# Optimization experiments

Measured on AMD Instinct MI355X. Metric: run time of the kernel, lower is better.

The kernel has to match this reference:

```python
import jax, jax.numpy as jnp
import numpy as np
from jax import lax

MU = 0.1          # cfg MODEL.MU (FISTA step size)
LMBD = 0.1        # cfg MODEL.LAMBDA[0]
N_STEPS = 4       # cfg MODEL.NUM_LAYERS (unrolled FISTA iterations)
BN_EPS = 1e-5


def _norm_w(W):
    # DictBlock w_norm: each dictionary filter normalized to unit L2 norm.
    # torch does this under no_grad (in-place on .data), so the norm is a constant.
    n = jnp.sqrt(jnp.sum(W * W, axis=(1, 2, 3), keepdims=True))
    return W / lax.stop_gradient(n + 1e-12)


def _conv(x, W, stride, pad):
    return lax.conv_general_dilated(x, W, (stride, stride), [(pad, pad)] * 2,
                                    dimension_numbers=('NCHW', 'OIHW', 'NCHW'))


def _conv_t(z, W, stride, pad, out_pad):
    # torch conv_transpose2d(z, W, stride, padding=pad, output_padding=out_pad)
    k = W.shape[2]
    Wt = jnp.transpose(jnp.flip(W, (2, 3)), (1, 0, 2, 3))  # (in_ch, dict, k, k)
    p = k - 1 - pad
    return lax.conv_general_dilated(z, Wt, (1, 1), [(p, p + out_pad)] * 2,
                                    lhs_dilation=(stride, stride),
                                    dimension_numbers=('NCHW', 'OIHW', 'NCHW'))


def _shrink(c):
    # non-negative soft threshold: relu(c - lmbd*step)
    return jax.nn.relu(c - LMBD * MU)


def _dict_conv(x, W, stride):
    # Unrolled FISTA sparse coding: min_c 0.5||x - W^T c||^2 + lmbd||c||_1, c>=0
    W = _norm_w(W)
    out_pad = stride - 1
    c = _shrink(MU * _conv(x, W, stride, 1))
    c_pre = jnp.zeros_like(c)
    t = 1.0
    for _ in range(N_STEPS - 1):
        t_next = (1.0 + float(np.sqrt(1.0 + 4.0 * t * t))) / 2.0
        a = c + ((t - 1.0) / t_next) * (c - c_pre)
        c_pre = c
        r = x - _conv_t(a, W, stride, 1, out_pad)       # reconstruction residual
        c = _shrink(a + MU * _conv(r, W, stride, 1))    # proximal gradient step
        t = t_next
    return c


def _bn(x, g, b, m, v):
    # eval-mode BatchNorm2d with running stats
    scale = g * lax.rsqrt(v + BN_EPS)
    return (x - m[None, :, None, None]) * scale[None, :, None, None] + b[None, :, None, None]


def setup_inputs() -> dict:
    key = jax.random.key(0)
    ks = jax.random.split(key, 12)
    N, Cin, Cout, H = 32, 128, 256, 56
    x = jax.random.normal(ks[0], (N, Cin, H, H), jnp.float32)
    def unit_norm(W):
        return W / (jnp.sqrt(jnp.sum(W * W, axis=(1, 2, 3), keepdims=True)) + 1e-12)
    W1 = unit_norm(jax.random.normal(ks[1], (Cout, Cin, 3, 3), jnp.float32))
    W2 = unit_norm(jax.random.normal(ks[2], (Cout, Cout, 3, 3), jnp.float32))
    Wsc = jax.random.normal(ks[3], (Cout, Cin, 1, 1), jnp.float32) * 0.05
    def bn(k):
        k1, k2, k3, k4 = jax.random.split(k, 4)
        g = 1.0 + 0.1 * jax.random.normal(k1, (Cout,), jnp.float32)
        b = 0.1 * jax.random.normal(k2, (Cout,), jnp.float32)
        m = 0.1 * jax.random.normal(k3, (Cout,), jnp.float32)
        v = 0.5 + jax.random.uniform(k4, (Cout,), jnp.float32)
        return g, b, m, v
    bn1_g, bn1_b, bn1_m, bn1_v = bn(ks[4])
    bn2_g, bn2_b, bn2_m, bn2_v = bn(ks[5])
    bnsc_g, bnsc_b, bnsc_m, bnsc_v = bn(ks[6])
    return dict(x=x, W1=W1, W2=W2, Wsc=Wsc,
                bn1_g=bn1_g, bn1_b=bn1_b, bn1_m=bn1_m, bn1_v=bn1_v,
                bn2_g=bn2_g, bn2_b=bn2_b, bn2_m=bn2_m, bn2_v=bn2_v,
                bnsc_g=bnsc_g, bnsc_b=bnsc_b, bnsc_m=bnsc_m, bnsc_v=bnsc_v)


def reference(x, W1, W2, Wsc,
              bn1_g, bn1_b, bn1_m, bn1_v,
              bn2_g, bn2_b, bn2_m, bn2_v,
              bnsc_g, bnsc_b, bnsc_m, bnsc_v):
    out = _bn(_dict_conv(x, W1, 2), bn1_g, bn1_b, bn1_m, bn1_v)
    out = _bn(_dict_conv(out, W2, 1), bn2_g, bn2_b, bn2_m, bn2_v)
    sc = _bn(_conv(x, Wsc, 2, 0), bnsc_g, bnsc_b, bnsc_m, bnsc_v)
    return jax.nn.relu(out + sc)
```

## Files before the change

### kernel.cpp

```cpp
#include <hip/hip_runtime.h>
#include <math.h>

#define MU_F 0.1f
#define SHRINK_F 0.01f
#define BN_EPS_F 1e-5f

typedef _Float16 half_t;
typedef _Float16 half8 __attribute__((ext_vector_type(8)));
typedef float f32x4 __attribute__((ext_vector_type(4)));

__device__ __forceinline__ void gll16(const half_t* g, half_t* l) {
    __builtin_amdgcn_global_load_lds(
        (const __attribute__((address_space(1))) void*)g,
        (__attribute__((address_space(3))) void*)l, 16, 0, 0);
}

#define VM_WAIT_BARRIER(N) do {                                   \
    asm volatile("s_waitcnt vmcnt(" #N ")" ::: "memory");         \
    __builtin_amdgcn_s_barrier();                                 \
    __builtin_amdgcn_sched_barrier(0);                            \
} while (0)

template<int KS, int S, int PAD, int MODE>
__global__ __launch_bounds__(256, 2)
void conv_big(const half_t* __restrict__ Ag, const half_t* __restrict__ Xh,
              float* __restrict__ outF, half_t* __restrict__ outH,
              const half_t* __restrict__ auxH, const float* __restrict__ auxF,
              int CA, int Cout, int Hin, int Win, int Hout, int Wout, int ptiles,
              float alpha, float beta, float delta, int relu1,
              const float* __restrict__ pscale, const float* __restrict__ pbias,
              const float* __restrict__ aux3, int relu2,
              const half_t* __restrict__ zpg, int edge_defer,
              float* __restrict__ out2F)
{
    __shared__ __align__(16) half_t sm[4 * 8192];

    const int tid = threadIdx.x;
    const int wv = tid >> 6, ln = tid & 63;
    const int co0 = blockIdx.y * 128;
    const int wco = (wv & 1) * 64, wpx = (wv >> 1) * 64;

    int bx;
    {
        const int nwg = gridDim.x;
        const int q = nwg >> 3, r8 = nwg & 7;
        const int xcd = blockIdx.x & 7, idx = blockIdx.x >> 3;
        bx = (xcd < r8 ? xcd * (q + 1) : r8 * (q + 1) + (xcd - r8) * q) + idx;
    }
    const int p0 = bx * 128;
    (void)ptiles;

    const int PHW1 = Hout * Wout;
    const int NPX  = PHW1 * 32;
    const int K9   = KS * KS * CA;

    const int r  = tid >> 2;
    const int s4 = tid & 3;
    const int sw = (s4 ^ ((r >> 1) & 3)) << 3;

    const size_t abase0 = (size_t)(co0 + r     ) * K9;
    const size_t abase1 = (size_t)(co0 + r + 64) * K9;

    int bph[2], bpw[2]; bool bval[2]; size_t bnb[2];
#pragma unroll
    for (int i = 0; i < 2; ++i) {
        int px = p0 + i * 64 + r;
        bval[i] = px < NPX;
        int pc = bval[i] ? px : 0;
        int n2 = pc / PHW1; int rem = pc - n2 * PHW1;
        int ph = rem / Wout;
        bph[i] = ph; bpw[i] = rem - ph * Wout;
        bnb[i] = (size_t)n2 * Hin * Win;
    }

    const int cpt = CA >> 5;
    const int lgc = (cpt == 8) ? 3 : 2;
    const int ntap = KS * KS;
    const int total = ntap << lgc;

    auto issue = [&](int flat, half_t* dst) {
        const int ci = flat & (cpt - 1);
        const int ti = flat >> lgc;
        int kh, kw;
        if (KS == 3) {
            kh = (ti * 11) >> 5; kw = ti - 3 * kh;
        } else { kh = 0; kw = 0; }
        const int c0 = ci << 5;
        const size_t koff = (size_t)(kh * KS + kw) * CA + c0 + sw;
        gll16(Ag + abase0 + koff, dst +        tid * 8);
        gll16(Ag + abase1 + koff, dst + 2048 + tid * 8);
#pragma unroll
        for (int i = 0; i < 2; ++i) {
            int hh, ww2; bool ok = bval[i];
            if (MODE == 0) {
                hh = bph[i] * S - PAD + kh; ww2 = bpw[i] * S - PAD + kw;
                ok = ok && (unsigned)hh < (unsigned)Hin && (unsigned)ww2 < (unsigned)Win;
            } else {
                hh = bph[i] + PAD - kh; ww2 = bpw[i] + PAD - kw;
                ok = ok && (unsigned)hh < (unsigned)Hin && (unsigned)ww2 < (unsigned)Win;
            }
            const half_t* src = ok
                ? Xh + (bnb[i] + (size_t)(hh * Win + ww2)) * CA + c0 + sw
                : zpg;
            gll16(src, dst + 4096 + i * 2048 + tid * 8);
        }
    };

    f32x4 acc[4][4] = {};

    issue(0, sm);
    issue(1, sm + 8192);
    issue(2, sm + 16384);
    VM_WAIT_BARRIER(8);

    const int fr = ln & 15, q8 = ln >> 4;
    const int sx = (q8 ^ ((fr >> 1) & 3)) << 3;
    const int rdA = (wco + fr) * 32 + sx;
    const int rdB = (128 + wpx + fr) * 32 + sx;

    for (int k = 0; k < total; ++k) {
        half_t* bufr = sm + (k & 3) * 8192;
        if (k + 3 < total)
            issue(k + 3, sm + ((k + 3) & 3) * 8192);
        half8 fa[4], fb[4];
#pragma unroll
        for (int m = 0; m < 4; ++m)
            fa[m] = *(const half8*)(bufr + rdA + m * 512);
#pragma unroll
        for (int t2 = 0; t2 < 4; ++t2)
            fb[t2] = *(const half8*)(bufr + rdB + t2 * 512);
#pragma unroll
        for (int m = 0; m < 4; ++m)
#pragma unroll
            for (int t2 = 0; t2 < 4; ++t2)
                acc[m][t2] = __builtin_amdgcn_mfma_f32_16x16x32_f16(fa[m], fb[t2], acc[m][t2], 0, 0, 0);
        if (k + 3 < total)      VM_WAIT_BARRIER(8);
        else if (k + 2 < total) VM_WAIT_BARRIER(4);
        else if (k + 1 < total) VM_WAIT_BARRIER(0);
    }

    const int rg = ln >> 4;
#pragma unroll
    for (int t = 0; t < 4; ++t) {
        int px = p0 + wpx + t * 16 + fr;
        if (px >= NPX) continue;
        int n2 = px / PHW1; int rem = px - n2 * PHW1;
        int oh = rem / Wout, ow = rem - oh * Wout;
        size_t ghwc = ((size_t)(n2 * Hout + oh) * Wout + ow) * Cout;
        bool defer = edge_defer && (oh == 0 || ow == 0);
#pragma unroll
        for (int m = 0; m < 4; ++m) {
#pragma unroll
            for (int rr = 0; rr < 4; ++rr) {
                int co_l = co0 + wco + m * 16 + rg * 4 + rr;
                size_t fidx = ((size_t)(n2 * Cout + co_l) * Hout + oh) * Wout + ow;
                float av = alpha * acc[m][t][rr];
                if (out2F) out2F[fidx] = av;
                float v = av + delta;
                if (auxH) v += beta * (float)auxH[ghwc + co_l];
                if (auxF) v += beta * auxF[fidx];
                if (!defer) {
                    if (relu1) v = fmaxf(v, 0.f);
                    if (pscale) v = pscale[co_l] * v + pbias[co_l];
                    if (aux3) v += aux3[fidx];
                    if (relu2) v = fmaxf(v, 0.f);
                }
                if (outH) outH[ghwc + co_l] = (half_t)v;
                else      outF[fidx] = v;
            }
        }
    }
}

template<int KT>
__global__ __launch_bounds__(256)
void pack_w(const float* __restrict__ W, half_t* __restrict__ Wh,
            half_t* __restrict__ WTh, int Cin, int Cout, int do_norm)
{
    __shared__ float red[256];
    int co = blockIdx.x, tid = threadIdx.x;
    int CK = Cin * KT;
    const float* w = W + (size_t)co * CK;
    float inv = 1.f;
    if (do_norm) {
        float s = 0.f;
        for (int i = tid; i < CK; i += 256) { float v = w[i]; s += v * v; }
        red[tid] = s; __syncthreads();
        for (int o = 128; o > 0; o >>= 1) {
            if (tid < o) red[tid] += red[tid + o];
            __syncthreads();
        }
        inv = 1.f / (sqrtf(red[0]) + 1e-12f);
    }
    for (int i = tid; i < CK; i += 256) {
        int ci = i / KT, tap = i - ci * KT;
        half_t h = (half_t)(w[i] * inv);
        Wh[((size_t)co * KT + tap) * Cin + ci] = h;
        if (WTh) WTh[((size_t)ci * KT + tap) * Cout + co] = h;
    }
}

__global__ __launch_bounds__(256)
void gram_kernel(const half_t* __restrict__ Wh, half_t* __restrict__ Gp,
                 half_t* __restrict__ ChT, half_t* __restrict__ CwT,
                 half_t* __restrict__ CcT)
{
    __shared__ float Wa[9 * 128];
    int co = blockIdx.x, b = threadIdx.x;
    for (int i = b; i < 9 * 128; i += 256) Wa[i] = (float)Wh[(size_t)co * 9 * 128 + i];
    __syncthreads();
    const half_t* Wb = Wh + (size_t)b * 9 * 128;
    auto dot = [&](int tA, int tB) {
        float s = 0.f;
        for (int c = 0; c < 128; ++c) s += Wa[tA * 128 + c] * (float)Wb[tB * 128 + c];
        return s;
    };
    auto lo = [](int t) { return (t == 2) ? 2 : 0; };
    auto hi = [](int t) { return (t == 1) ? 3 : ((t == 2) ? 3 : 1); };
    for (int th = 0; th < 3; ++th)
        for (int tw = 0; tw < 3; ++tw) {
            float s = 0.f;
            for (int kh = lo(th); kh < hi(th); ++kh)
                for (int kw = lo(tw); kw < hi(tw); ++kw)
                    s += dot(kh * 3 + kw, (kh + 2 - 2 * th) * 3 + (kw + 2 - 2 * tw));
            Gp[((size_t)co * 9 + th * 3 + tw) * 256 + b] = (half_t)s;
        }
    for (int tw = 0; tw < 3; ++tw) {
        float s = 0.f, s2 = 0.f;
        for (int k = lo(tw); k < hi(tw); ++k) {
            s  += dot(k, k + 2 - 2 * tw);
            s2 += dot(k * 3, (k + 2 - 2 * tw) * 3);
        }
        ChT[((size_t)tw * 256 + b) * 256 + co] = (half_t)s;
        CwT[((size_t)tw * 256 + b) * 256 + co] = (half_t)s2;
    }
    CcT[(size_t)b * 256 + co] = (half_t)dot(0, 0);
}

__global__ __launch_bounds__(256)
void edge_fix(const half_t* __restrict__ a, half_t* out,
              const half_t* __restrict__ ChT, const half_t* __restrict__ CwT,
              const half_t* __restrict__ CcT,
              const float* __restrict__ ps, const float* __restrict__ pb)
{
    int i = blockIdx.x, n = blockIdx.y, co = threadIdx.x;
    int oh, ow;
    if (i < 28) { oh = 0; ow = i; } else { oh = i - 27; ow = 0; }
    float corr = 0.f;
    if (oh == 0) {
        for (int kw = 0; kw < 3; ++kw) {
            int pw = ow - 1 + kw;
            if ((unsigned)pw < 28u) {
                const half_t* ap = a + ((size_t)(n * 28 + 0) * 28 + pw) * 256;
                const half_t* cp = ChT + (size_t)kw * 256 * 256 + co;
                for (int b2 = 0; b2 < 256; ++b2)
                    corr += (float)cp[(size_t)b2 * 256] * (float)ap[b2];
            }
        }
    }
    if (ow == 0) {
        for (int kh = 0; kh < 3; ++kh) {
            int ph = oh - 1 + kh;
            if ((unsigned)ph < 28u) {
                const half_t* ap = a + ((size_t)(n * 28 + ph) * 28 + 0) * 256;
                const half_t* cp = CwT + (size_t)kh * 256 * 256 + co;
                for (int b2 = 0; b2 < 256; ++b2)
                    corr += (float)cp[(size_t)b2 * 256] * (float)ap[b2];
            }
        }
    }
    if (oh == 0 && ow == 0) {
        const half_t* ap = a + ((size_t)(n * 28) * 28) * 256;
        for (int b2 = 0; b2 < 256; ++b2)
            corr -= (float)CcT[(size_t)b2 * 256 + co] * (float)ap[b2];
    }
    size_t idx = ((size_t)(n * 28 + oh) * 28 + ow) * 256 + co;
    float v = (float)out[idx] + MU_F * corr;
    v = fmaxf(v, 0.f);
    if (ps) v = ps[co] * v + pb[co];
    out[idx] = (half_t)v;
}

__global__ __launch_bounds__(256)
void tx_kernel(const float* __restrict__ x, half_t* __restrict__ xTh)
{
    __shared__ __align__(16) half_t tl[56 * 136];
    int h = blockIdx.x, n = blockIdx.y, tid = threadIdx.x;
    for (int it = 0; it < 28; ++it) {
        int id = tid + it * 256;
        int c = id / 56, w0 = id - c * 56;
        tl[w0 * 136 + c] = (half_t)x[(((size_t)n * 128 + c) * 56 + h) * 56 + w0];
    }
    __syncthreads();
    if (tid < 224) {
        int w0 = tid >> 2, part = tid & 3;
        size_t base = (((size_t)n * 56 + h) * 56 + w0) * 128 + part * 32;
#pragma unroll
        for (int j = 0; j < 4; ++j)
            *(half8*)(xTh + base + j * 8) = *(const half8*)(tl + w0 * 136 + part * 32 + j * 8);
    }
}

__global__ __launch_bounds__(256)
void comb_kernel(const half_t* __restrict__ c, const half_t* __restrict__ p,
                 half_t* __restrict__ a, float w1, float w2, int n8)
{
    int i = blockIdx.x * 256 + threadIdx.x;
    if (i >= n8) return;
    half8 cv = ((const half8*)c)[i];
    half8 pv = ((const half8*)p)[i];
    half8 rres;
#pragma unroll
    for (int j = 0; j < 8; ++j) rres[j] = (half_t)(w1 * (float)cv[j] + w2 * (float)pv[j]);
    ((half8*)a)[i] = rres;
}

__global__ __launch_bounds__(256)
void bn_prep_kernel(const float* __restrict__ g, const float* __restrict__ b,
                    const float* __restrict__ m, const float* __restrict__ v,
                    float* __restrict__ s, float* __restrict__ t, int C)
{
    int i = blockIdx.x * 256 + threadIdx.x;
    if (i < C) {
        float sc = g[i] * rsqrtf(v[i] + BN_EPS_F);
        s[i] = sc; t[i] = b[i] - m[i] * sc;
    }
}

__global__ __launch_bounds__(128)
void zfill_kernel(half_t* __restrict__ p)
{
    p[threadIdx.x] = (half_t)0.f;
}

extern "C" void kernel_launch(void* const* d_in, const int* in_sizes, int n_in,
                              void* d_out, int out_size, void* d_ws, size_t ws_size,
                              hipStream_t stream)
{
    (void)in_sizes; (void)n_in; (void)out_size;
    const float* x    = (const float*)d_in[0];
    const float* W1   = (const float*)d_in[1];
    const float* W2   = (const float*)d_in[2];
    const float* Wsc  = (const float*)d_in[3];
    const float* bn1g = (const float*)d_in[4];
    const float* bn1b = (const float*)d_in[5];
    const float* bn1m = (const float*)d_in[6];
    const float* bn1v = (const float*)d_in[7];
    const float* bn2g = (const float*)d_in[8];
    const float* bn2b = (const float*)d_in[9];
    const float* bn2m = (const float*)d_in[10];
    const float* bn2v = (const float*)d_in[11];
    const float* bscg = (const float*)d_in[12];
    const float* bscb = (const float*)d_in[13];
    const float* bscm = (const float*)d_in[14];
    const float* bscv = (const float*)d_in[15];

    const size_t NB = (size_t)32 * 256 * 28 * 28;
    const size_t NX = (size_t)32 * 128 * 56 * 56;

    char* base = (char*)d_ws;
    size_t off = 0;
    auto alloc = [&](size_t nbytes) -> void* {
        void* r = base + off;
        off = (off + nbytes + 255) & ~(size_t)255;
        return r;
    };
    half_t* Wh1  = (half_t*)alloc(294912 * 2);
    half_t* WTh1 = (half_t*)alloc(294912 * 2);
    half_t* Wh2  = (half_t*)alloc(589824 * 2);
    half_t* WTh2 = (half_t*)alloc(589824 * 2);
    half_t* Wsch = (half_t*)alloc(32768 * 2);
    half_t* Gph  = (half_t*)alloc(589824 * 2);
    half_t* ChT  = (half_t*)alloc(196608 * 2);
    half_t* CwT  = (half_t*)alloc(196608 * 2);
    half_t* CcT  = (half_t*)alloc(65536 * 2);
    float* bn1s = (float*)alloc(256 * 4);  float* bn1t = (float*)alloc(256 * 4);
    float* bn2s = (float*)alloc(256 * 4);  float* bn2t = (float*)alloc(256 * 4);
    float* bscs = (float*)alloc(256 * 4);  float* bsct = (float*)alloc(256 * 4);
    half_t* zpg  = (half_t*)alloc(256);
    half_t* xTh  = (half_t*)alloc(NX * 2);
    half_t* Pa   = (half_t*)alloc(NB * 2);
    half_t* Pb   = (half_t*)alloc(NB * 2);
    half_t* Pc   = (half_t*)alloc(NB * 2);
    half_t* Py   = (half_t*)alloc(NB * 2);
    half_t* r28h = (half_t*)alloc(NB * 2);
    float*  scF  = (float*)alloc(NB * 4);
    if (off > ws_size) return;
    (void)WTh1;

    float*  cxF = (float*)Py;
    half_t* Pd  = (half_t*)xTh;

    float* outp = (float*)d_out;

    double t = 1.0; float al[3];
    for (int i = 0; i < 3; ++i) {
        double tn = (1.0 + sqrt(1.0 + 4.0 * t * t)) / 2.0;
        al[i] = (float)((t - 1.0) / tn); t = tn;
    }

    const dim3 blk(256);
    const dim3 cblk(256);
    const dim3 gB(196, 2, 1);
    const dim3 gE(55, 32, 1);
    const int n8 = (int)(NB / 8);
    const dim3 gC((n8 + 255) / 256);
    const float* NF = nullptr;
    const half_t* NH = nullptr;
    float* NFo = nullptr;
    half_t* NHo = nullptr;

    pack_w<9><<<256, blk, 0, stream>>>(W1, Wh1, nullptr, 128, 256, 1);
    pack_w<9><<<256, blk, 0, stream>>>(W2, Wh2, WTh2, 256, 256, 1);
    pack_w<1><<<256, blk, 0, stream>>>(Wsc, Wsch, nullptr, 128, 256, 0);
    gram_kernel<<<256, blk, 0, stream>>>(Wh1, Gph, ChT, CwT, CcT);
    bn_prep_kernel<<<1, blk, 0, stream>>>(bn1g, bn1b, bn1m, bn1v, bn1s, bn1t, 256);
    bn_prep_kernel<<<1, blk, 0, stream>>>(bn2g, bn2b, bn2m, bn2v, bn2s, bn2t, 256);
    bn_prep_kernel<<<1, blk, 0, stream>>>(bscg, bscb, bscm, bscv, bscs, bsct, 256);
    zfill_kernel<<<1, dim3(128), 0, stream>>>(zpg);
    tx_kernel<<<dim3(56, 32), blk, 0, stream>>>(x, xTh);

    conv_big<3,2,1,0><<<gB, cblk, 0, stream>>>(Wh1, xTh, NFo, Pa, NH, NF,
        128, 256, 56, 56, 28, 28, 196, MU_F, 0.f, -SHRINK_F, 1, NF, NF, NF, 0, zpg, 0, cxF);
    conv_big<1,2,0,0><<<gB, cblk, 0, stream>>>(Wsch, xTh, scF, NHo, NH, NF,
        128, 256, 56, 56, 28, 28, 196, 1.f, 0.f, 0.f, 0, bscs, bsct, NF, 0, zpg, 0, NFo);

    conv_big<3,1,1,0><<<gB, cblk, 0, stream>>>(Gph, Pa, NFo, Pb, Pa, cxF,
        256, 256, 28, 28, 28, 28, 196, -MU_F, 1.f, -SHRINK_F, 1, NF, NF, NF, 0, zpg, 1, NFo);
    edge_fix<<<gE, cblk, 0, stream>>>(Pa, Pb, ChT, CwT, CcT, NF, NF);

    comb_kernel<<<gC, blk, 0, stream>>>(Pb, Pa, Pc, 1.f + al[1], -al[1], n8);
    conv_big<3,1,1,0><<<gB, cblk, 0, stream>>>(Gph, Pc, NFo, Pa, Pc, cxF,
        256, 256, 28, 28, 28, 28, 196, -MU_F, 1.f, -SHRINK_F, 1, NF, NF, NF, 0, zpg, 1, NFo);
    edge_fix<<<gE, cblk, 0, stream>>>(Pc, Pa, ChT, CwT, CcT, NF, NF);

    comb_kernel<<<gC, blk, 0, stream>>>(Pa, Pb, Pc, 1.f + al[2], -al[2], n8);
    conv_big<3,1,1,0><<<gB, cblk, 0, stream>>>(Gph, Pc, NFo, Pb, Pc, cxF,
        256, 256, 28, 28, 28, 28, 196, -MU_F, 1.f, -SHRINK_F, 1, bn1s, bn1t, NF, 0, zpg, 1, NFo);
    edge_fix<<<gE, cblk, 0, stream>>>(Pc, Pb, ChT, CwT, CcT, bn1s, bn1t);

    conv_big<3,1,1,0><<<gB, cblk, 0, stream>>>(Wh2, Pb, NFo, Pa, NH, NF,
        256, 256, 28, 28, 28, 28, 196, MU_F, 0.f, -SHRINK_F, 1, NF, NF, NF, 0, zpg, 0, NFo);

    conv_big<3,1,1,1><<<gB, cblk, 0, stream>>>(WTh2, Pa, NFo, r28h, Pb, NF,
        256, 256, 28, 28, 28, 28, 196, -1.f, 1.f, 0.f, 0, NF, NF, NF, 0, zpg, 0, NFo);
    conv_big<3,1,1,0><<<gB, cblk, 0, stream>>>(Wh2, r28h, NFo, Pd, Pa, NF,
        256, 256, 28, 28, 28, 28, 196, MU_F, 1.f, -SHRINK_F, 1, NF, NF, NF, 0, zpg, 0, NFo);

    comb_kernel<<<gC, blk, 0, stream>>>(Pd, Pa, Pc, 1.f + al[1], -al[1], n8);
    conv_big<3,1,1,1><<<gB, cblk, 0, stream>>>(WTh2, Pc, NFo, r28h, Pb, NF,
        256, 256, 28, 28, 28, 28, 196, -1.f, 1.f, 0.f, 0, NF, NF, NF, 0, zpg, 0, NFo);
    conv_big<3,1,1,0><<<gB, cblk, 0, stream>>>(Wh2, r28h, NFo, Pa, Pc, NF,
        256, 256, 28, 28, 28, 28, 196, MU_F, 1.f, -SHRINK_F, 1, NF, NF, NF, 0, zpg, 0, NFo);

    comb_kernel<<<gC, blk, 0, stream>>>(Pa, Pd, Pc, 1.f + al[2], -al[2], n8);
    conv_big<3,1,1,1><<<gB, cblk, 0, stream>>>(WTh2, Pc, NFo, r28h, Pb, NF,
        256, 256, 28, 28, 28, 28, 196, -1.f, 1.f, 0.f, 0, NF, NF, NF, 0, zpg, 0, NFo);
    conv_big<3,1,1,0><<<gB, cblk, 0, stream>>>(Wh2, r28h, outp, NHo, Pc, NF,
        256, 256, 28, 28, 28, 28, 196, MU_F, 1.f, -SHRINK_F, 1, bn2s, bn2t, scF, 1, zpg, 0, NFo);
}
```

Measured before the change: 1.317 ms.

## Load activation operand directly to registers and repack weights into K-chunked layout

The conv GEMM kernel no longer stages the pixel (B) operand through shared memory. Each lane now gathers its half8 fragments straight from global memory into double-buffered registers, while only the weight (A) tile still goes through a 3-slot LDS ring. Weights and the Gram matrix are repacked into a [k-chunk][tap][cout][32] layout so each A tile is one contiguous block, and a separate raw-layout pack feeds the Gram computation. This cuts LDS use and barrier traffic per step, at the cost of uncoalesced per-lane global gathers and a shallower prefetch depth.

Result: slower. 1.623 ms (+23.3%).

```diff
diff --git a/kernel.cpp b/kernel.cpp
--- a/kernel.cpp
+++ b/kernel.cpp
@@ -33,12 +33,13 @@
               const half_t* __restrict__ zpg, int edge_defer,
               float* __restrict__ out2F)
 {
-    __shared__ __align__(16) half_t sm[4 * 8192];
+    __shared__ __align__(16) half_t sm[3 * 4096];
 
     const int tid = threadIdx.x;
     const int wv = tid >> 6, ln = tid & 63;
     const int co0 = blockIdx.y * 128;
     const int wco = (wv & 1) * 64, wpx = (wv >> 1) * 64;
+    (void)ptiles;
 
     int bx;
     {
@@ -48,104 +49,95 @@
         bx = (xcd < r8 ? xcd * (q + 1) : r8 * (q + 1) + (xcd - r8) * q) + idx;
     }
     const int p0 = bx * 128;
-    (void)ptiles;
 
     const int PHW1 = Hout * Wout;
     const int NPX  = PHW1 * 32;
-    const int K9   = KS * KS * CA;
-
-    const int r  = tid >> 2;
-    const int s4 = tid & 3;
-    const int sw = (s4 ^ ((r >> 1) & 3)) << 3;
-
-    const size_t abase0 = (size_t)(co0 + r     ) * K9;
-    const size_t abase1 = (size_t)(co0 + r + 64) * K9;
-
-    int bph[2], bpw[2]; bool bval[2]; size_t bnb[2];
-#pragma unroll
-    for (int i = 0; i < 2; ++i) {
-        int px = p0 + i * 64 + r;
-        bval[i] = px < NPX;
-        int pc = bval[i] ? px : 0;
-        int n2 = pc / PHW1; int rem = pc - n2 * PHW1;
-        int ph = rem / Wout;
-        bph[i] = ph; bpw[i] = rem - ph * Wout;
-        bnb[i] = (size_t)n2 * Hin * Win;
-    }
-
-    const int cpt = CA >> 5;
-    const int lgc = (cpt == 8) ? 3 : 2;
-    const int ntap = KS * KS;
-    const int total = ntap << lgc;
-
-    auto issue = [&](int flat, half_t* dst) {
-        const int ci = flat & (cpt - 1);
-        const int ti = flat >> lgc;
-        int kh, kw;
-        if (KS == 3) {
-            kh = (ti * 11) >> 5; kw = ti - 3 * kh;
-        } else { kh = 0; kw = 0; }
-        const int c0 = ci << 5;
-        const size_t koff = (size_t)(kh * KS + kw) * CA + c0 + sw;
-        gll16(Ag + abase0 + koff, dst +        tid * 8);
-        gll16(Ag + abase1 + koff, dst + 2048 + tid * 8);
-#pragma unroll
-        for (int i = 0; i < 2; ++i) {
-            int hh, ww2; bool ok = bval[i];
-            if (MODE == 0) {
-                hh = bph[i] * S - PAD + kh; ww2 = bpw[i] * S - PAD + kw;
-                ok = ok && (unsigned)hh < (unsigned)Hin && (unsigned)ww2 < (unsigned)Win;
-            } else {
-                hh = bph[i] + PAD - kh; ww2 = bpw[i] + PAD - kw;
-                ok = ok && (unsigned)hh < (unsigned)Hin && (unsigned)ww2 < (unsigned)Win;
-            }
-            const half_t* src = ok
-                ? Xh + (bnb[i] + (size_t)(hh * Win + ww2)) * CA + c0 + sw
-                : zpg;
-            gll16(src, dst + 4096 + i * 2048 + tid * 8);
-        }
+
+    const int r   = tid >> 2;
+    const int s4  = tid & 3;
+    const int asl = (s4 ^ ((r >> 1) & 3)) << 3;
+
+    const int fr = ln & 15, q8 = ln >> 4;
+    const int koh = q8 * 8;
+    const int sx  = (q8 ^ ((fr >> 1) & 3)) << 3;
+    const int rdA = (wco + fr) * 32 + sx;
+
+    const int cpt   = CA >> 5;
+    const int ntap  = KS * KS;
+    const int total = ntap * cpt;
+
+    int eph[4], epw[4], en2[4]; size_t ebase[4]; bool evalid[4];
+#pragma unroll
+    for (int t2 = 0; t2 < 4; ++t2) {
+        int px = p0 + wpx + t2 * 16 + fr;
+        evalid[t2] = px < NPX;
+        int pc = evalid[t2] ? px : 0;
+        en2[t2] = pc / PHW1; int rem = pc - en2[t2] * PHW1;
+        eph[t2] = rem / Wout; epw[t2] = rem - eph[t2] * Wout;
+        ebase[t2] = (size_t)en2[t2] * Hin * Win;
+    }
+
+    auto issueA = [&](int flat, half_t* dst) {
+        const size_t base = ((size_t)flat * Cout + co0) * 32;
+        gll16(Ag + base + (size_t)r * 32 + asl,        dst +        tid * 8);
+        gll16(Ag + base + (size_t)(r + 64) * 32 + asl, dst + 2048 + tid * 8);
     };
 
+    auto loadB = [&](int flat, half8 (&rb)[4]) {
+        int cc, ti;
+        if (KS == 1) { cc = flat; ti = 0; }
+        else         { cc = (flat * 57) >> 9; ti = flat - 9 * cc; }
+        const int kh = (KS == 3) ? ((ti * 11) >> 5) : 0;
+        const int kw = (KS == 3) ? (ti - 3 * kh) : 0;
+        const int c0h = (cc << 5) + koh;
+#pragma unroll
+        for (int t2 = 0; t2 < 4; ++t2) {
+            int ihh, iww; bool ok = evalid[t2];
+            if (MODE == 0) { ihh = eph[t2] * S - PAD + kh; iww = epw[t2] * S - PAD + kw; }
+            else           { ihh = eph[t2] + PAD - kh;     iww = epw[t2] + PAD - kw; }
+            ok = ok && (unsigned)ihh < (unsigned)Hin && (unsigned)iww < (unsigned)Win;
+            long long soff = ((long long)ebase[t2] + (long long)ihh * Win + iww) * CA + c0h;
+            const half_t* p = ok ? (Xh + soff) : zpg;
+            rb[t2] = *(const half8*)p;
+        }
+    };
+
     f32x4 acc[4][4] = {};
-
-    issue(0, sm);
-    issue(1, sm + 8192);
-    issue(2, sm + 16384);
-    VM_WAIT_BARRIER(8);
-
-    const int fr = ln & 15, q8 = ln >> 4;
-    const int sx = (q8 ^ ((fr >> 1) & 3)) << 3;
-    const int rdA = (wco + fr) * 32 + sx;
-    const int rdB = (128 + wpx + fr) * 32 + sx;
-
-    for (int k = 0; k < total; ++k) {
-        half_t* bufr = sm + (k & 3) * 8192;
-        if (k + 3 < total)
-            issue(k + 3, sm + ((k + 3) & 3) * 8192);
-        half8 fa[4], fb[4];
+    half8 rb0[4], rb1[4];
+
+    issueA(0, sm);
+    issueA(1, sm + 4096);
+    __builtin_amdgcn_sched_barrier(0);
+    loadB(0, rb0);
+    VM_WAIT_BARRIER(6);
+
+    auto step = [&](int k, half8 (&rbR)[4], half8 (&rbW)[4]) {
+        half_t* slot = sm + (k % 3) * 4096;
+        if (k + 2 < total) issueA(k + 2, sm + ((k + 2) % 3) * 4096);
+        __builtin_amdgcn_sched_barrier(0);
+        if (k + 1 < total) loadB(k + 1, rbW);
+        half8 fa[4];
 #pragma unroll
         for (int m = 0; m < 4; ++m)
-            fa[m] = *(const half8*)(bufr + rdA + m * 512);
-#pragma unroll
-        for (int t2 = 0; t2 < 4; ++t2)
-            fb[t2] = *(const half8*)(bufr + rdB + t2 * 512);
+            fa[m] = *(const half8*)(slot + rdA + m * 512);
 #pragma unroll
         for (int m = 0; m < 4; ++m)
 #pragma unroll
             for (int t2 = 0; t2 < 4; ++t2)
-                acc[m][t2] = __builtin_amdgcn_mfma_f32_16x16x32_f16(fa[m], fb[t2], acc[m][t2], 0, 0, 0);
-        if (k + 3 < total)      VM_WAIT_BARRIER(8);
-        else if (k + 2 < total) VM_WAIT_BARRIER(4);
-        else if (k + 1 < total) VM_WAIT_BARRIER(0);
+                acc[m][t2] = __builtin_amdgcn_mfma_f32_16x16x32_f16(fa[m], rbR[t2], acc[m][t2], 0, 0, 0);
+        if (k + 1 < total) VM_WAIT_BARRIER(6);
+    };
+
+    for (int k = 0; k < total; k += 2) {
+        step(k,     rb0, rb1);
+        step(k + 1, rb1, rb0);
     }
 
     const int rg = ln >> 4;
 #pragma unroll
     for (int t = 0; t < 4; ++t) {
-        int px = p0 + wpx + t * 16 + fr;
-        if (px >= NPX) continue;
-        int n2 = px / PHW1; int rem = px - n2 * PHW1;
-        int oh = rem / Wout, ow = rem - oh * Wout;
+        if (!evalid[t]) continue;
+        int oh = eph[t], ow = epw[t], n2 = en2[t];
         size_t ghwc = ((size_t)(n2 * Hout + oh) * Wout + ow) * Cout;
         bool defer = edge_defer && (oh == 0 || ow == 0);
 #pragma unroll
@@ -195,8 +187,8 @@
     for (int i = tid; i < CK; i += 256) {
         int ci = i / KT, tap = i - ci * KT;
         half_t h = (half_t)(w[i] * inv);
-        Wh[((size_t)co * KT + tap) * Cin + ci] = h;
-        if (WTh) WTh[((size_t)ci * KT + tap) * Cout + co] = h;
+        Wh[(((size_t)(ci >> 5) * KT + tap) * Cout + co) * 32 + (ci & 31)] = h;
+        if (WTh) WTh[(((size_t)(co >> 5) * KT + tap) * Cin + ci) * 32 + (co & 31)] = h;
     }
 }
 
@@ -223,7 +215,7 @@
             for (int kh = lo(th); kh < hi(th); ++kh)
                 for (int kw = lo(tw); kw < hi(tw); ++kw)
                     s += dot(kh * 3 + kw, (kh + 2 - 2 * th) * 3 + (kw + 2 - 2 * tw));
-            Gp[((size_t)co * 9 + th * 3 + tw) * 256 + b] = (half_t)s;
+            Gp[(((size_t)(b >> 5) * 9 + th * 3 + tw) * 256 + co) * 32 + (b & 31)] = (half_t)s;
         }
     for (int tw = 0; tw < 3; ++tw) {
         float s = 0.f, s2 = 0.f;
@@ -235,6 +227,26 @@
         CwT[((size_t)tw * 256 + b) * 256 + co] = (half_t)s2;
     }
     CcT[(size_t)b * 256 + co] = (half_t)dot(0, 0);
+}
+
+__global__ __launch_bounds__(256)
+void pack_raw(const float* __restrict__ W, half_t* __restrict__ Wr, int CK)
+{
+    __shared__ float red[256];
+    int co = blockIdx.x, tid = threadIdx.x;
+    const float* w = W + (size_t)co * CK;
+    float s = 0.f;
+    for (int i = tid; i < CK; i += 256) { float v = w[i]; s += v * v; }
+    red[tid] = s; __syncthreads();
+    for (int o = 128; o > 0; o >>= 1) {
+        if (tid < o) red[tid] += red[tid + o];
+        __syncthreads();
+    }
+    float inv = 1.f / (sqrtf(red[0]) + 1e-12f);
+    for (int i = tid; i < CK; i += 256) {
+        int ci = i / 9, tap = i - ci * 9;
+        Wr[((size_t)co * 9 + tap) * (CK / 9) + ci] = (half_t)(w[i] * inv);
+    }
 }
 
 __global__ __launch_bounds__(256)
@@ -366,7 +378,7 @@
         return r;
     };
     half_t* Wh1  = (half_t*)alloc(294912 * 2);
-    half_t* WTh1 = (half_t*)alloc(294912 * 2);
+    half_t* Wr1  = (half_t*)alloc(294912 * 2);
     half_t* Wh2  = (half_t*)alloc(589824 * 2);
     half_t* WTh2 = (half_t*)alloc(589824 * 2);
     half_t* Wsch = (half_t*)alloc(32768 * 2);
@@ -386,7 +398,6 @@
     half_t* r28h = (half_t*)alloc(NB * 2);
     float*  scF  = (float*)alloc(NB * 4);
     if (off > ws_size) return;
-    (void)WTh1;
 
     float*  cxF = (float*)Py;
     half_t* Pd  = (half_t*)xTh;
@@ -411,9 +422,10 @@
     half_t* NHo = nullptr;
 
     pack_w<9><<<256, blk, 0, stream>>>(W1, Wh1, nullptr, 128, 256, 1);
+    pack_raw<<<256, blk, 0, stream>>>(W1, Wr1, 128 * 9);
     pack_w<9><<<256, blk, 0, stream>>>(W2, Wh2, WTh2, 256, 256, 1);
     pack_w<1><<<256, blk, 0, stream>>>(Wsc, Wsch, nullptr, 128, 256, 0);
-    gram_kernel<<<256, blk, 0, stream>>>(Wh1, Gph, ChT, CwT, CcT);
+    gram_kernel<<<256, blk, 0, stream>>>(Wr1, Gph, ChT, CwT, CcT);
     bn_prep_kernel<<<1, blk, 0, stream>>>(bn1g, bn1b, bn1m, bn1v, bn1s, bn1t, 256);
     bn_prep_kernel<<<1, blk, 0, stream>>>(bn2g, bn2b, bn2m, bn2v, bn2s, bn2t, 256);
     bn_prep_kernel<<<1, blk, 0, stream>>>(bscg, bscb, bscm, bscv, bscs, bsct, 256);
```
